# Kernel optimization log

Measured on AMD Instinct MI355X. Metric: run time of the kernel, lower is better.

The kernel has to match this reference:

```python
import jax, jax.numpy as jnp
import numpy as np

ALPHA = 0.2  # LeakyReLU negative slope
NEG = -9e15

def _gat_head(Wh, a1, a2, adj_mask):
    # Wh: [N,O], a1/a2: [O], adj_mask: [N,N] bool
    e = jax.nn.leaky_relu(jnp.einsum('no,o->n', Wh, a1)[:, None]
                          + jnp.einsum('no,o->n', Wh, a2)[None, :], ALPHA)
    att = jax.nn.softmax(jnp.where(adj_mask, e, NEG), axis=-1)
    return att @ Wh  # [N,O]

def setup_inputs() -> dict:
    key = jax.random.key(0)
    ks = jax.random.split(key, 6)
    N, F_IN, O, H, C = 4096, 512, 64, 8, 16
    x = jax.random.normal(ks[0], (N, F_IN), jnp.float32)
    adj = jax.random.randint(ks[1], (N, N), 0, 2, jnp.int32)
    W = jax.random.normal(ks[2], (H, F_IN, O), jnp.float32) * 0.05
    a = jax.random.normal(ks[3], (H, 2 * O), jnp.float32) * 0.05
    W_out = jax.random.normal(ks[4], (H * O, C), jnp.float32) * 0.05
    a_out = jax.random.normal(ks[5], (2 * C,), jnp.float32) * 0.05
    return {'x': x, 'adj': adj, 'W': W, 'a': a, 'W_out': W_out, 'a_out': a_out}

def reference(x, adj, W, a, W_out, a_out):
    N = x.shape[0]
    H, _, O = W.shape
    C = W_out.shape[1]
    mask = adj > 0  # [N,N]
    # multi-head attention layer (vmapped over heads)
    Wh = jnp.einsum('nf,hfo->hno', x, W)  # [H,N,O]
    a1, a2 = a[:, :O], a[:, O:]
    h_heads = jax.vmap(_gat_head, in_axes=(0, 0, 0, None))(Wh, a1, a2, mask)  # [H,N,O]
    h = jax.nn.elu(h_heads)  # concat=True -> elu per head
    h = jnp.transpose(h, (1, 0, 2)).reshape(N, H * O)  # concat heads
    # output attention layer (concat=False)
    Wh_o = h @ W_out  # [N,C]
    out = _gat_head(Wh_o, a_out[:C], a_out[C:], mask)  # [N,C]
    out = jax.nn.elu(out)
    return jax.nn.log_softmax(out, axis=1)
```

## Files before the change

### kernel.cpp

```cpp
#include <hip/hip_runtime.h>


typedef _Float16 h2 __attribute__((ext_vector_type(2)));
typedef _Float16 half8 __attribute__((ext_vector_type(8)));
typedef __attribute__((ext_vector_type(4))) float f32x4;
typedef unsigned long long u64;
typedef unsigned short u16;
typedef unsigned int u32;

__device__ __forceinline__ u16 f2h(float f){
  union { _Float16 h; u16 u; } c; c.h = (_Float16)f; return c.u;
}
__device__ __forceinline__ h2 u2h2(u32 u){ union { u32 u; h2 h; } c; c.u = u; return c.h; }
__device__ __forceinline__ u32 h22u(h2 h){ union { u32 u; h2 h; } c; c.h = h; return c.u; }
__device__ __forceinline__ half8 pk2h8(uint4 v){ union { uint4 u; half8 h; } c; c.u = v; return c.h; }

__device__ __forceinline__ void async16(void* lds, const void* g){
  __builtin_amdgcn_global_load_lds((const __attribute__((address_space(1))) u32*)g,
                                   (__attribute__((address_space(3))) u32*)lds, 16, 0, 0);
}
__device__ __forceinline__ void async4(void* lds, const void* g){
  __builtin_amdgcn_global_load_lds((const __attribute__((address_space(1))) u32*)g,
                                   (__attribute__((address_space(3))) u32*)lds, 4, 0, 0);
}

__global__ __launch_bounds__(256) void k_wpack(const float* __restrict__ W,
                                               u16* __restrict__ Wb16){
  int t = blockIdx.x * 256 + threadIdx.x;
  int o   = t & 63;
  int fgb = (t >> 6) & 63;
  int h   = t >> 12;
  const float* src = W + ((size_t)h * 512 + fgb * 8) * 64 + o;
  u32 pk[4];
  #pragma unroll
  for (int p = 0; p < 4; ++p)
    pk[p] = (u32)f2h(src[(2 * p) * 64]) | ((u32)f2h(src[(2 * p + 1) * 64]) << 16);
  *(uint4*)(Wb16 + ((size_t)h * 4096 + fgb * 64 + o) * 8) = *(uint4*)pk;
}

__global__ __launch_bounds__(256) void k_gemm1(const float* __restrict__ x,
                                               const u16* __restrict__ Wb16,
                                               const float* __restrict__ av,
                                               const int* __restrict__ adj,
                                               u16* __restrict__ whB,
                                               u64* __restrict__ bits_t,
                                               float* __restrict__ r1,
                                               u16* __restrict__ e21h, u16* __restrict__ e202h){
  __shared__ u16 tr[4096];
  int h    = blockIdx.y;
  int bx   = blockIdx.x;
  int tid  = threadIdx.x;
  int lane = tid & 63;
  int wv   = tid >> 6;

  if (bx >= 64){
    int B = h * 64 + (bx - 64);
    int uid0 = B * 512 + wv * 128;
    for (int k = 0; k < 128; k += 8){
      int v[8];
      #pragma unroll
      for (int q = 0; q < 8; ++q){
        int uid = uid0 + k + q;
        v[q] = adj[(size_t)(uid >> 6) * 4096 + ((uid & 63) << 6) + lane];
      }
      u64 m[8];
      #pragma unroll
      for (int q = 0; q < 8; ++q) m[q] = __ballot(v[q] != 0);
      if (lane == 0){
        #pragma unroll
        for (int q = 0; q < 8; ++q){
          int uid = uid0 + k + q;
          bits_t[(size_t)(uid & 63) * 4096 + (uid >> 6)] = m[q];
        }
      }
    }
    return;
  }

  int row16 = lane & 15, grp = lane >> 4;
  int n0 = bx * 64;
  int n0w = n0 + wv * 16;
  const u16* wb = Wb16 + (size_t)h * 32768;

  f32x4 acc[4] = {};
  #pragma unroll 4
  for (int ks = 0; ks < 16; ++ks){
    int fgb = ks * 4 + grp;
    const float* xs = x + (size_t)(n0w + row16) * 512 + fgb * 8;
    float4 xv0 = ((const float4*)xs)[0];
    float4 xv1 = ((const float4*)xs)[1];
    u32 ax[4];
    ax[0] = (u32)f2h(xv0.x) | ((u32)f2h(xv0.y) << 16);
    ax[1] = (u32)f2h(xv0.z) | ((u32)f2h(xv0.w) << 16);
    ax[2] = (u32)f2h(xv1.x) | ((u32)f2h(xv1.y) << 16);
    ax[3] = (u32)f2h(xv1.z) | ((u32)f2h(xv1.w) << 16);
    half8 af = pk2h8(*(uint4*)ax);
    #pragma unroll
    for (int nt = 0; nt < 4; ++nt){
      half8 bf = *(const half8*)(wb + ((size_t)fgb * 64 + nt * 16 + row16) * 8);
      acc[nt] = __builtin_amdgcn_mfma_f32_16x16x32_f16(af, bf, acc[nt], 0, 0, 0);
    }
  }
  float a1v[4], a2v[4];
  #pragma unroll
  for (int nt = 0; nt < 4; ++nt){
    a1v[nt] = av[h * 128 + nt * 16 + row16];
    a2v[nt] = av[h * 128 + 64 + nt * 16 + row16];
  }
  #pragma unroll
  for (int r = 0; r < 4; ++r){
    float p1 = acc[0][r]*a1v[0] + acc[1][r]*a1v[1] + acc[2][r]*a1v[2] + acc[3][r]*a1v[3];
    float p2 = acc[0][r]*a2v[0] + acc[1][r]*a2v[1] + acc[2][r]*a2v[2] + acc[3][r]*a2v[3];
    #pragma unroll
    for (int d = 1; d < 16; d <<= 1){ p1 += __shfl_xor(p1, d, 64); p2 += __shfl_xor(p2, d, 64); }
    if (row16 == 0){
      int idx = h * 4096 + n0w + grp * 4 + r;
      r1[idx]    = __expf(-0.8f * p1);
      e21h[idx]  = f2h(__expf(p2));
      e202h[idx] = f2h(__expf(0.2f * p2));
    }
  }
  #pragma unroll
  for (int nt = 0; nt < 4; ++nt)
    #pragma unroll
    for (int r = 0; r < 4; ++r){
      int jl = wv * 16 + grp * 4 + r;
      int o  = nt * 16 + row16;
      tr[((jl >> 3) * 64 + o) * 8 + (jl & 7)] = f2h(acc[nt][r]);
    }
  __syncthreads();
  u16* dst = whB + (size_t)h * 262144 + (size_t)n0 * 64;
  #pragma unroll
  for (int q = 0; q < 2; ++q)
    *(uint4*)(dst + (tid * 2 + q) * 8) = *(const uint4*)(tr + (tid * 2 + q) * 8);
}

__global__ __launch_bounds__(256) void k_att1(const u16* __restrict__ whB,
                                              const u64* __restrict__ bits_t,
                                              const float* __restrict__ r1,
                                              const u16* __restrict__ e21h, const u16* __restrict__ e202h,
                                              u16* __restrict__ pnum, float* __restrict__ pden){
  __shared__ u16  smB[2][4096];
  __shared__ u32  smT[2][2][64];
  __shared__ u32  smLut[4];
  int h     = blockIdx.y;
  int iblk  = blockIdx.x;
  int split = blockIdx.z;
  int lane = threadIdx.x & 63;
  int wv   = threadIdx.x >> 6;
  int row16 = lane & 15, grp = lane >> 4;
  if (threadIdx.x < 4)
    smLut[threadIdx.x] = ((threadIdx.x & 1) ? 0xFFFFu : 0u) | ((threadIdx.x & 2) ? 0xFFFF0000u : 0u);
  int i = iblk * 64 + wv * 16 + row16;
  int hoff = h * 4096;
  u32 rb = (u32)f2h(r1[hoff + i]); rb |= rb << 16;
  h2 rr = u2h2(rb);
  const u16* whBh = whB + (size_t)h * 262144;
  int jbeg = split * 1024;

  half8 bden;
  {
    u32 z[4] = {0,0,0,0};
    if (row16 == 0){ z[0]=0x3C003C00u; z[1]=0x3C003C00u; z[2]=0x3C003C00u; z[3]=0x3C003C00u; }
    bden = pk2h8(*(uint4*)z);
  }

  auto stage = [&](int bb, int j0){
    const char* g = (const char*)whBh + (size_t)j0 * 128 + wv * 2048 + lane * 16;
    char* l = (char*)(&smB[bb][0]) + wv * 2048;
    async16(l, g);
    async16(l + 1024, g + 1024);
    if (wv == 0)      async4(&smT[bb][0][0], (const char*)(e21h  + hoff + j0) + lane * 4);
    else if (wv == 1) async4(&smT[bb][1][0], (const char*)(e202h + hoff + j0) + lane * 4);
  };

  f32x4 acc[4] = {};
  f32x4 accden = {};
  stage(0, jbeg);
  for (int c = 0; c < 16; ++c){
    int bb = c & 1;
    u64 mrow = bits_t[(size_t)(split * 16 + c) * 4096 + i];
    __syncthreads();
    if (c < 15) stage(bb ^ 1, jbeg + (c + 1) * 64);
    #pragma unroll
    for (int ks = 0; ks < 2; ++ks){
      uint4 e1q = *(const uint4*)((const char*)&smT[bb][0][0] + ks * 64 + grp * 16);
      uint4 e2q = *(const uint4*)((const char*)&smT[bb][1][0] + ks * 64 + grp * 16);
      u32 es[4] = {e1q.x, e1q.y, e1q.z, e1q.w};
      u32 gs[4] = {e2q.x, e2q.y, e2q.z, e2q.w};
      const u16* bbase = &smB[bb][(ks * 4 + grp) * 512];
      half8 bf0 = *(const half8*)(bbase + (0 * 16 + row16) * 8);
      half8 bf1 = *(const half8*)(bbase + (1 * 16 + row16) * 8);
      half8 bf2 = *(const half8*)(bbase + (2 * 16 + row16) * 8);
      half8 bf3 = *(const half8*)(bbase + (3 * 16 + row16) * 8);
      u32 mb = ((u32)(mrow >> (ks * 32)) >> (grp * 8)) & 0xffu;
      u32 pk[4];
      #pragma unroll
      for (int t2i = 0; t2i < 4; ++t2i){
        h2 w = __builtin_elementwise_max(u2h2(es[t2i]), rr * u2h2(gs[t2i]));
        pk[t2i] = h22u(w) & smLut[(mb >> (2 * t2i)) & 3u];
      }
      half8 af = pk2h8(*(uint4*)pk);
      acc[0] = __builtin_amdgcn_mfma_f32_16x16x32_f16(af, bf0, acc[0], 0, 0, 0);
      acc[1] = __builtin_amdgcn_mfma_f32_16x16x32_f16(af, bf1, acc[1], 0, 0, 0);
      acc[2] = __builtin_amdgcn_mfma_f32_16x16x32_f16(af, bf2, acc[2], 0, 0, 0);
      acc[3] = __builtin_amdgcn_mfma_f32_16x16x32_f16(af, bf3, acc[3], 0, 0, 0);
      accden = __builtin_amdgcn_mfma_f32_16x16x32_f16(af, bden, accden, 0, 0, 0);
    }
  }

  #pragma unroll
  for (int r4 = 0; r4 < 4; ++r4){
    int n = iblk * 64 + wv * 16 + grp * 4 + r4;
    if (row16 == 0)
      pden[((size_t)split * 8 + h) * 4096 + n] = accden[r4];
    u16* dst = pnum + ((size_t)split * 4096 + n) * 512 + h * 64 + row16;
    #pragma unroll
    for (int nt = 0; nt < 4; ++nt)
      dst[nt * 16] = f2h(acc[nt][r4]);
  }
}

__global__ __launch_bounds__(256) void k_gemm2(const u16* __restrict__ pnum,
                                               const float* __restrict__ pden,
                                               const float* __restrict__ Wout,
                                               const float* __restrict__ aout,
                                               u16* __restrict__ whoB,
                                               float* __restrict__ r1o,
                                               u16* __restrict__ e21oh, u16* __restrict__ e202oh){
  __shared__ float Wl[8192];
  __shared__ float hrow[16 * 516];
  __shared__ float sden[128];
  int n0 = blockIdx.x * 16;
  for (int t = threadIdx.x; t < 8192; t += 256) Wl[t] = Wout[t];
  if (threadIdx.x < 128){
    int hh = threadIdx.x >> 4, nn = threadIdx.x & 15;
    float d = 0.f;
    #pragma unroll
    for (int s = 0; s < 4; ++s) d += pden[((size_t)s * 8 + hh) * 4096 + n0 + nn];
    sden[threadIdx.x] = d;
  }
  __syncthreads();
  {
    int nn = threadIdx.x >> 4;
    int fc = threadIdx.x & 15;
    int f0 = fc * 32;
    int hh = fc >> 1;
    float dinv = 1.f / sden[hh * 16 + nn];
    float v[32];
    #pragma unroll
    for (int k = 0; k < 32; ++k) v[k] = 0.f;
    #pragma unroll
    for (int s = 0; s < 4; ++s){
      const u16* p = pnum + ((size_t)s * 4096 + n0 + nn) * 512 + f0;
      #pragma unroll
      for (int q = 0; q < 4; ++q){
        uint4 raw = *(const uint4*)(p + q * 8);
        u32 rw[4] = {raw.x, raw.y, raw.z, raw.w};
        #pragma unroll
        for (int d2 = 0; d2 < 4; ++d2){
          h2 dh = u2h2(rw[d2]);
          v[q * 8 + d2 * 2]     += (float)dh.x;
          v[q * 8 + d2 * 2 + 1] += (float)dh.y;
        }
      }
    }
    #pragma unroll
    for (int k = 0; k < 32; ++k){
      float val = v[k] * dinv;
      val = val > 0.f ? val : (__expf(val) - 1.f);
      hrow[nn * 516 + f0 + k] = val;
    }
  }
  __syncthreads();
  int c  = threadIdx.x & 15;
  int rl = threadIdx.x >> 4;
  int n = n0 + rl;
  const float4* hr = (const float4*)(hrow + rl * 516);
  float acc = 0.f;
  #pragma unroll 8
  for (int f4 = 0; f4 < 128; ++f4){
    float4 hv = hr[f4];
    int f = f4 * 4;
    acc += hv.x * Wl[f * 16 + c] + hv.y * Wl[(f + 1) * 16 + c]
         + hv.z * Wl[(f + 2) * 16 + c] + hv.w * Wl[(f + 3) * 16 + c];
  }
  whoB[((size_t)(n >> 3) * 16 + c) * 8 + (n & 7)] = f2h(acc);
  float p1 = acc * aout[c], p2 = acc * aout[16 + c];
  #pragma unroll
  for (int d = 1; d < 16; d <<= 1){ p1 += __shfl_xor(p1, d, 64); p2 += __shfl_xor(p2, d, 64); }
  if (c == 0){
    r1o[n]    = __expf(-0.8f * p1);
    e21oh[n]  = f2h(__expf(p2));
    e202oh[n] = f2h(__expf(0.2f * p2));
  }
}

__global__ __launch_bounds__(256) void k_att2(const u16* __restrict__ whoB,
                                              const u64* __restrict__ bits_t,
                                              const float* __restrict__ r1o,
                                              const u16* __restrict__ e21oh, const u16* __restrict__ e202oh,
                                              float* __restrict__ pnum, float* __restrict__ pden){
  __shared__ u32 smLut[4];
  int iblk  = blockIdx.x;
  int split = blockIdx.y;
  int lane = threadIdx.x & 63;
  int wv   = threadIdx.x >> 6;
  int row16 = lane & 15, grp = lane >> 4;
  if (threadIdx.x < 4)
    smLut[threadIdx.x] = ((threadIdx.x & 1) ? 0xFFFFu : 0u) | ((threadIdx.x & 2) ? 0xFFFF0000u : 0u);
  __syncthreads();
  int i = iblk * 64 + wv * 16 + row16;
  u32 rb = (u32)f2h(r1o[i]); rb |= rb << 16;
  h2 rr = u2h2(rb);
  int jbeg = split * 256;
  half8 bden;
  {
    u32 z[4] = {0,0,0,0};
    if (row16 == 0){ z[0]=0x3C003C00u; z[1]=0x3C003C00u; z[2]=0x3C003C00u; z[3]=0x3C003C00u; }
    bden = pk2h8(*(uint4*)z);
  }

  f32x4 acc = {};
  f32x4 accden = {};
  #pragma unroll
  for (int c = 0; c < 4; ++c){
    int j0 = jbeg + c * 64;
    u64 mrow = bits_t[(size_t)(split * 4 + c) * 4096 + i];
    #pragma unroll
    for (int ks = 0; ks < 2; ++ks){
      int sb = (j0 >> 3) + ks * 4 + grp;
      half8 bf = *(const half8*)(whoB + ((size_t)sb * 16 + row16) * 8);
      uint4 e1q = *(const uint4*)(e21oh  + j0 + ks * 32 + grp * 8);
      uint4 e2q = *(const uint4*)(e202oh + j0 + ks * 32 + grp * 8);
      u32 es[4] = {e1q.x, e1q.y, e1q.z, e1q.w};
      u32 gs[4] = {e2q.x, e2q.y, e2q.z, e2q.w};
      u32 mb = ((u32)(mrow >> (ks * 32)) >> (grp * 8)) & 0xffu;
      u32 pk[4];
      #pragma unroll
      for (int t2i = 0; t2i < 4; ++t2i){
        h2 w = __builtin_elementwise_max(u2h2(es[t2i]), rr * u2h2(gs[t2i]));
        pk[t2i] = h22u(w) & smLut[(mb >> (2 * t2i)) & 3u];
      }
      half8 af = pk2h8(*(uint4*)pk);
      acc    = __builtin_amdgcn_mfma_f32_16x16x32_f16(af, bf, acc, 0, 0, 0);
      accden = __builtin_amdgcn_mfma_f32_16x16x32_f16(af, bden, accden, 0, 0, 0);
    }
  }
  #pragma unroll
  for (int r4 = 0; r4 < 4; ++r4){
    int n = iblk * 64 + wv * 16 + grp * 4 + r4;
    if (row16 == 0)
      pden[(size_t)n * 16 + split] = accden[r4];
    pnum[((size_t)n * 16 + split) * 16 + row16] = acc[r4];
  }
}

__global__ __launch_bounds__(256) void k_final(const float* __restrict__ pnum,
                                               const float* __restrict__ pden,
                                               float* __restrict__ out){
  int tid = blockIdx.x * 256 + threadIdx.x;
  int c = tid & 15;
  int n = tid >> 4;
  float num = 0.f, den = 0.f;
  #pragma unroll
  for (int s = 0; s < 16; ++s){
    num += pnum[((size_t)n * 16 + s) * 16 + c];
    den += pden[(size_t)n * 16 + s];
  }
  float v = num / den;
  v = v > 0.f ? v : (__expf(v) - 1.f);
  float m = v;
  #pragma unroll
  for (int d = 1; d < 16; d <<= 1) m = fmaxf(m, __shfl_xor(m, d, 64));
  float es = __expf(v - m), ss = es;
  #pragma unroll
  for (int d = 1; d < 16; d <<= 1) ss += __shfl_xor(ss, d, 64);
  out[(size_t)n * 16 + c] = v - m - __logf(ss);
}

extern "C" void kernel_launch(void* const* d_in, const int* in_sizes, int n_in,
                              void* d_out, int out_size, void* d_ws, size_t ws_size,
                              hipStream_t stream){
  (void)in_sizes; (void)n_in; (void)out_size; (void)ws_size;
  const float* x    = (const float*)d_in[0];
  const int*   adj  = (const int*)d_in[1];
  const float* W    = (const float*)d_in[2];
  const float* av   = (const float*)d_in[3];
  const float* Wout = (const float*)d_in[4];
  const float* aout = (const float*)d_in[5];
  float* out = (float*)d_out;
  char* ws = (char*)d_ws;

  u64*  bits_t  = (u64*)(ws + 0x0000000);
  u16*  whB     = (u16*)(ws + 0x0200000);
  float* r1     = (float*)(ws + 0x0600000);
  u16*  e21h    = (u16*)(ws + 0x0620000);
  u16*  e202h   = (u16*)(ws + 0x0630000);
  u16*  pnum1   = (u16*)(ws + 0x0680000);
  float* pden1  = (float*)(ws + 0x1680000);
  u16*  whoB    = (u16*)(ws + 0x1700000);
  float* r1o    = (float*)(ws + 0x1720000);
  u16*  e21oh   = (u16*)(ws + 0x1724000);
  u16*  e202oh  = (u16*)(ws + 0x1726000);
  float* pnum2  = (float*)(ws + 0x1730000);
  float* pden2  = (float*)(ws + 0x1B30000);
  u16*  Wb16    = (u16*)(ws + 0x1730000);

  k_wpack<<<dim3(128), dim3(256), 0, stream>>>(W, Wb16);
  k_gemm1<<<dim3(128, 8), dim3(256), 0, stream>>>(x, Wb16, av, adj, whB, bits_t, r1, e21h, e202h);
  k_att1<<<dim3(64, 8, 4), dim3(256), 0, stream>>>(whB, bits_t, r1, e21h, e202h, pnum1, pden1);
  k_gemm2<<<dim3(256), dim3(256), 0, stream>>>(pnum1, pden1, Wout, aout, whoB, r1o, e21oh, e202oh);
  k_att2<<<dim3(64, 16), dim3(256), 0, stream>>>(whoB, bits_t, r1o, e21oh, e202oh, pnum2, pden2);
  k_final<<<dim3(256), dim3(256), 0, stream>>>(pnum2, pden2, out);
}
```

Baseline: 175.3 us.

## Pre-pack x to fp16 MFMA layout and restructure gemm2 as one row per wave

```diff
diff --git a/kernel.cpp b/kernel.cpp
--- a/kernel.cpp
+++ b/kernel.cpp
@@ -24,21 +24,44 @@
                                    (__attribute__((address_space(3))) u32*)lds, 4, 0, 0);
 }
 
-__global__ __launch_bounds__(256) void k_wpack(const float* __restrict__ W,
-                                               u16* __restrict__ Wb16){
-  int t = blockIdx.x * 256 + threadIdx.x;
-  int o   = t & 63;
-  int fgb = (t >> 6) & 63;
-  int h   = t >> 12;
-  const float* src = W + ((size_t)h * 512 + fgb * 8) * 64 + o;
-  u32 pk[4];
-  #pragma unroll
-  for (int p = 0; p < 4; ++p)
-    pk[p] = (u32)f2h(src[(2 * p) * 64]) | ((u32)f2h(src[(2 * p + 1) * 64]) << 16);
-  *(uint4*)(Wb16 + ((size_t)h * 4096 + fgb * 64 + o) * 8) = *(uint4*)pk;
-}
-
-__global__ __launch_bounds__(256) void k_gemm1(const float* __restrict__ x,
+__global__ __launch_bounds__(256) void k_prep(const float* __restrict__ W,
+                                              const float* __restrict__ x,
+                                              u16* __restrict__ Wb16,
+                                              u16* __restrict__ xA){
+  int bx = blockIdx.x;
+  int tid = threadIdx.x;
+  if (bx < 256){
+    int ngrp = bx;
+    int row16 = tid & 15;
+    int fq    = tid >> 4;
+    const float* xs = x + ((size_t)ngrp * 16 + row16) * 512;
+    #pragma unroll
+    for (int it = 0; it < 4; ++it){
+      int fgb = fq * 4 + it;
+      float4 a0 = *(const float4*)(xs + fgb * 8);
+      float4 a1 = *(const float4*)(xs + fgb * 8 + 4);
+      u32 pk[4];
+      pk[0] = (u32)f2h(a0.x) | ((u32)f2h(a0.y) << 16);
+      pk[1] = (u32)f2h(a0.z) | ((u32)f2h(a0.w) << 16);
+      pk[2] = (u32)f2h(a1.x) | ((u32)f2h(a1.y) << 16);
+      pk[3] = (u32)f2h(a1.z) | ((u32)f2h(a1.w) << 16);
+      *(uint4*)(xA + (((size_t)ngrp * 64 + fgb) * 16 + row16) * 8) = *(uint4*)pk;
+    }
+  } else {
+    int t = (bx - 256) * 256 + tid;
+    int o   = t & 63;
+    int fgb = (t >> 6) & 63;
+    int h   = t >> 12;
+    const float* src = W + ((size_t)h * 512 + fgb * 8) * 64 + o;
+    u32 pk[4];
+    #pragma unroll
+    for (int p = 0; p < 4; ++p)
+      pk[p] = (u32)f2h(src[(2 * p) * 64]) | ((u32)f2h(src[(2 * p + 1) * 64]) << 16);
+    *(uint4*)(Wb16 + ((size_t)h * 4096 + fgb * 64 + o) * 8) = *(uint4*)pk;
+  }
+}
+
+__global__ __launch_bounds__(256) void k_gemm1(const u16* __restrict__ xA,
                                                const u16* __restrict__ Wb16,
                                                const float* __restrict__ av,
                                                const int* __restrict__ adj,
@@ -81,20 +104,13 @@
   int n0 = bx * 64;
   int n0w = n0 + wv * 16;
   const u16* wb = Wb16 + (size_t)h * 32768;
+  const u16* xa = xA + (size_t)(bx * 4 + wv) * 8192;
 
   f32x4 acc[4] = {};
   #pragma unroll 4
   for (int ks = 0; ks < 16; ++ks){
     int fgb = ks * 4 + grp;
-    const float* xs = x + (size_t)(n0w + row16) * 512 + fgb * 8;
-    float4 xv0 = ((const float4*)xs)[0];
-    float4 xv1 = ((const float4*)xs)[1];
-    u32 ax[4];
-    ax[0] = (u32)f2h(xv0.x) | ((u32)f2h(xv0.y) << 16);
-    ax[1] = (u32)f2h(xv0.z) | ((u32)f2h(xv0.w) << 16);
-    ax[2] = (u32)f2h(xv1.x) | ((u32)f2h(xv1.y) << 16);
-    ax[3] = (u32)f2h(xv1.z) | ((u32)f2h(xv1.w) << 16);
-    half8 af = pk2h8(*(uint4*)ax);
+    half8 af = *(const half8*)(xa + ((size_t)fgb * 16 + row16) * 8);
     #pragma unroll
     for (int nt = 0; nt < 4; ++nt){
       half8 bf = *(const half8*)(wb + ((size_t)fgb * 64 + nt * 16 + row16) * 8);
@@ -228,68 +244,57 @@
                                                u16* __restrict__ whoB,
                                                float* __restrict__ r1o,
                                                u16* __restrict__ e21oh, u16* __restrict__ e202oh){
-  __shared__ float Wl[8192];
-  __shared__ float hrow[16 * 516];
-  __shared__ float sden[128];
-  int n0 = blockIdx.x * 16;
-  for (int t = threadIdx.x; t < 8192; t += 256) Wl[t] = Wout[t];
-  if (threadIdx.x < 128){
-    int hh = threadIdx.x >> 4, nn = threadIdx.x & 15;
-    float d = 0.f;
-    #pragma unroll
-    for (int s = 0; s < 4; ++s) d += pden[((size_t)s * 8 + hh) * 4096 + n0 + nn];
-    sden[threadIdx.x] = d;
-  }
-  __syncthreads();
-  {
-    int nn = threadIdx.x >> 4;
-    int fc = threadIdx.x & 15;
-    int f0 = fc * 32;
-    int hh = fc >> 1;
-    float dinv = 1.f / sden[hh * 16 + nn];
-    float v[32];
-    #pragma unroll
-    for (int k = 0; k < 32; ++k) v[k] = 0.f;
-    #pragma unroll
-    for (int s = 0; s < 4; ++s){
-      const u16* p = pnum + ((size_t)s * 4096 + n0 + nn) * 512 + f0;
-      #pragma unroll
-      for (int q = 0; q < 4; ++q){
-        uint4 raw = *(const uint4*)(p + q * 8);
-        u32 rw[4] = {raw.x, raw.y, raw.z, raw.w};
-        #pragma unroll
-        for (int d2 = 0; d2 < 4; ++d2){
-          h2 dh = u2h2(rw[d2]);
-          v[q * 8 + d2 * 2]     += (float)dh.x;
-          v[q * 8 + d2 * 2 + 1] += (float)dh.y;
-        }
-      }
-    }
-    #pragma unroll
-    for (int k = 0; k < 32; ++k){
-      float val = v[k] * dinv;
-      val = val > 0.f ? val : (__expf(val) - 1.f);
-      hrow[nn * 516 + f0 + k] = val;
-    }
-  }
-  __syncthreads();
-  int c  = threadIdx.x & 15;
-  int rl = threadIdx.x >> 4;
-  int n = n0 + rl;
-  const float4* hr = (const float4*)(hrow + rl * 516);
-  float acc = 0.f;
-  #pragma unroll 8
-  for (int f4 = 0; f4 < 128; ++f4){
-    float4 hv = hr[f4];
-    int f = f4 * 4;
-    acc += hv.x * Wl[f * 16 + c] + hv.y * Wl[(f + 1) * 16 + c]
-         + hv.z * Wl[(f + 2) * 16 + c] + hv.w * Wl[(f + 3) * 16 + c];
-  }
-  whoB[((size_t)(n >> 3) * 16 + c) * 8 + (n & 7)] = f2h(acc);
-  float p1 = acc * aout[c], p2 = acc * aout[16 + c];
-  #pragma unroll
-  for (int d = 1; d < 16; d <<= 1){ p1 += __shfl_xor(p1, d, 64); p2 += __shfl_xor(p2, d, 64); }
-  if (c == 0){
+  int wv = threadIdx.x >> 6;
+  int l  = threadIdx.x & 63;
+  int n  = blockIdx.x * 4 + wv;
+  int f0 = l * 8;
+  int hh = l >> 3;
+  float v[8] = {0.f,0.f,0.f,0.f,0.f,0.f,0.f,0.f};
+  float d = 0.f;
+  #pragma unroll
+  for (int s = 0; s < 4; ++s){
+    uint4 raw = *(const uint4*)(pnum + ((size_t)s * 4096 + n) * 512 + f0);
+    u32 rw[4] = {raw.x, raw.y, raw.z, raw.w};
+    #pragma unroll
+    for (int q = 0; q < 4; ++q){
+      h2 dh = u2h2(rw[q]);
+      v[q * 2]     += (float)dh.x;
+      v[q * 2 + 1] += (float)dh.y;
+    }
+    d += pden[((size_t)s * 8 + hh) * 4096 + n];
+  }
+  float dinv = 1.f / d;
+  #pragma unroll
+  for (int k = 0; k < 8; ++k){
+    float val = v[k] * dinv;
+    v[k] = val > 0.f ? val : (__expf(val) - 1.f);
+  }
+  float pc[16];
+  #pragma unroll
+  for (int c = 0; c < 16; ++c) pc[c] = 0.f;
+  const float4* wr = (const float4*)(Wout + (size_t)f0 * 16);
+  #pragma unroll
+  for (int k = 0; k < 8; ++k){
+    float4 w0 = wr[k * 4 + 0], w1 = wr[k * 4 + 1], w2 = wr[k * 4 + 2], w3 = wr[k * 4 + 3];
+    float vk = v[k];
+    pc[0]  += vk * w0.x;  pc[1]  += vk * w0.y;  pc[2]  += vk * w0.z;  pc[3]  += vk * w0.w;
+    pc[4]  += vk * w1.x;  pc[5]  += vk * w1.y;  pc[6]  += vk * w1.z;  pc[7]  += vk * w1.w;
+    pc[8]  += vk * w2.x;  pc[9]  += vk * w2.y;  pc[10] += vk * w2.z;  pc[11] += vk * w2.w;
+    pc[12] += vk * w3.x;  pc[13] += vk * w3.y;  pc[14] += vk * w3.z;  pc[15] += vk * w3.w;
+  }
+  #pragma unroll
+  for (int c = 0; c < 16; ++c)
+    #pragma unroll
+    for (int dd = 1; dd < 64; dd <<= 1)
+      pc[c] += __shfl_xor(pc[c], dd, 64);
+  if (l == 0){
+    float p1 = 0.f, p2 = 0.f;
+    #pragma unroll
+    for (int c = 0; c < 16; ++c){
+      whoB[((size_t)(n >> 3) * 16 + c) * 8 + (n & 7)] = f2h(pc[c]);
+      p1 += pc[c] * aout[c];
+      p2 += pc[c] * aout[16 + c];
+    }
     r1o[n]    = __expf(-0.8f * p1);
     e21oh[n]  = f2h(__expf(p2));
     e202oh[n] = f2h(__expf(0.2f * p2));
@@ -406,11 +411,12 @@
   float* pnum2  = (float*)(ws + 0x1730000);
   float* pden2  = (float*)(ws + 0x1B30000);
   u16*  Wb16    = (u16*)(ws + 0x1730000);
-
-  k_wpack<<<dim3(128), dim3(256), 0, stream>>>(W, Wb16);
-  k_gemm1<<<dim3(128, 8), dim3(256), 0, stream>>>(x, Wb16, av, adj, whB, bits_t, r1, e21h, e202h);
+  u16*  xA      = (u16*)(ws + 0x0680000);
+
+  k_prep<<<dim3(384), dim3(256), 0, stream>>>(W, x, Wb16, xA);
+  k_gemm1<<<dim3(128, 8), dim3(256), 0, stream>>>(xA, Wb16, av, adj, whB, bits_t, r1, e21h, e202h);
   k_att1<<<dim3(64, 8, 4), dim3(256), 0, stream>>>(whB, bits_t, r1, e21h, e202h, pnum1, pden1);
-  k_gemm2<<<dim3(256), dim3(256), 0, stream>>>(pnum1, pden1, Wout, aout, whoB, r1o, e21oh, e202oh);
+  k_gemm2<<<dim3(1024), dim3(256), 0, stream>>>(pnum1, pden1, Wout, aout, whoB, r1o, e21oh, e202oh);
   k_att2<<<dim3(64, 16), dim3(256), 0, stream>>>(whoB, bits_t, r1o, e21oh, e202oh, pnum2, pden2);
   k_final<<<dim3(256), dim3(256), 0, stream>>>(pnum2, pden2, out);
 }
```

Result: slower. 186.0 us (+6.1%).

## Restructure gemm2 to four rows per block with split-K and direct W_out reads

Applied to the files above, without the earlier changes.

```diff
diff --git a/kernel.cpp b/kernel.cpp
--- a/kernel.cpp
+++ b/kernel.cpp
@@ -228,68 +228,59 @@
                                                u16* __restrict__ whoB,
                                                float* __restrict__ r1o,
                                                u16* __restrict__ e21oh, u16* __restrict__ e202oh){
-  __shared__ float Wl[8192];
-  __shared__ float hrow[16 * 516];
-  __shared__ float sden[128];
-  int n0 = blockIdx.x * 16;
-  for (int t = threadIdx.x; t < 8192; t += 256) Wl[t] = Wout[t];
-  if (threadIdx.x < 128){
-    int hh = threadIdx.x >> 4, nn = threadIdx.x & 15;
+  __shared__ float hrowf[4][512];
+  int n0  = blockIdx.x * 4;
+  int tid = threadIdx.x;
+  {
+    int nn = tid >> 6;
+    int fc = tid & 63;
+    int f0 = fc * 8;
+    int hh = fc >> 3;
+    int n  = n0 + nn;
+    float v[8] = {0.f,0.f,0.f,0.f,0.f,0.f,0.f,0.f};
     float d = 0.f;
     #pragma unroll
-    for (int s = 0; s < 4; ++s) d += pden[((size_t)s * 8 + hh) * 4096 + n0 + nn];
-    sden[threadIdx.x] = d;
-  }
-  __syncthreads();
-  {
-    int nn = threadIdx.x >> 4;
-    int fc = threadIdx.x & 15;
-    int f0 = fc * 32;
-    int hh = fc >> 1;
-    float dinv = 1.f / sden[hh * 16 + nn];
-    float v[32];
-    #pragma unroll
-    for (int k = 0; k < 32; ++k) v[k] = 0.f;
-    #pragma unroll
     for (int s = 0; s < 4; ++s){
-      const u16* p = pnum + ((size_t)s * 4096 + n0 + nn) * 512 + f0;
+      uint4 raw = *(const uint4*)(pnum + ((size_t)s * 4096 + n) * 512 + f0);
+      u32 rw[4] = {raw.x, raw.y, raw.z, raw.w};
       #pragma unroll
       for (int q = 0; q < 4; ++q){
-        uint4 raw = *(const uint4*)(p + q * 8);
-        u32 rw[4] = {raw.x, raw.y, raw.z, raw.w};
-        #pragma unroll
-        for (int d2 = 0; d2 < 4; ++d2){
-          h2 dh = u2h2(rw[d2]);
-          v[q * 8 + d2 * 2]     += (float)dh.x;
-          v[q * 8 + d2 * 2 + 1] += (float)dh.y;
-        }
+        h2 dh = u2h2(rw[q]);
+        v[q * 2]     += (float)dh.x;
+        v[q * 2 + 1] += (float)dh.y;
       }
-    }
-    #pragma unroll
-    for (int k = 0; k < 32; ++k){
+      d += pden[((size_t)s * 8 + hh) * 4096 + n];
+    }
+    float dinv = 1.f / d;
+    #pragma unroll
+    for (int k = 0; k < 8; ++k){
       float val = v[k] * dinv;
-      val = val > 0.f ? val : (__expf(val) - 1.f);
-      hrow[nn * 516 + f0 + k] = val;
+      hrowf[nn][f0 + k] = val > 0.f ? val : (__expf(val) - 1.f);
     }
   }
   __syncthreads();
-  int c  = threadIdx.x & 15;
-  int rl = threadIdx.x >> 4;
-  int n = n0 + rl;
-  const float4* hr = (const float4*)(hrow + rl * 516);
-  float acc = 0.f;
-  #pragma unroll 8
-  for (int f4 = 0; f4 < 128; ++f4){
-    float4 hv = hr[f4];
-    int f = f4 * 4;
-    acc += hv.x * Wl[f * 16 + c] + hv.y * Wl[(f + 1) * 16 + c]
-         + hv.z * Wl[(f + 2) * 16 + c] + hv.w * Wl[(f + 3) * 16 + c];
-  }
-  whoB[((size_t)(n >> 3) * 16 + c) * 8 + (n & 7)] = f2h(acc);
+  int rl = tid >> 6;
+  int kq = (tid >> 4) & 3;
+  int c  = tid & 15;
+  int n  = n0 + rl;
+  const float* hr = &hrowf[rl][kq * 128];
+  const float* wp = Wout + (size_t)(kq * 128) * 16 + c;
+  float a0 = 0.f, a1 = 0.f;
+  #pragma unroll 16
+  for (int f = 0; f < 128; f += 2){
+    a0 += hr[f]     * wp[f * 16];
+    a1 += hr[f + 1] * wp[f * 16 + 16];
+  }
+  float acc = a0 + a1;
+  acc += __shfl_xor(acc, 16, 64);
+  acc += __shfl_xor(acc, 32, 64);
+  int lane = tid & 63;
+  if ((lane >> 4) == 0)
+    whoB[((size_t)(n >> 3) * 16 + c) * 8 + (n & 7)] = f2h(acc);
   float p1 = acc * aout[c], p2 = acc * aout[16 + c];
   #pragma unroll
   for (int d = 1; d < 16; d <<= 1){ p1 += __shfl_xor(p1, d, 64); p2 += __shfl_xor(p2, d, 64); }
-  if (c == 0){
+  if (lane == 0){
     r1o[n]    = __expf(-0.8f * p1);
     e21oh[n]  = f2h(__expf(p2));
     e202oh[n] = f2h(__expf(0.2f * p2));
@@ -410,7 +401,7 @@
   k_wpack<<<dim3(128), dim3(256), 0, stream>>>(W, Wb16);
   k_gemm1<<<dim3(128, 8), dim3(256), 0, stream>>>(x, Wb16, av, adj, whB, bits_t, r1, e21h, e202h);
   k_att1<<<dim3(64, 8, 4), dim3(256), 0, stream>>>(whB, bits_t, r1, e21h, e202h, pnum1, pden1);
-  k_gemm2<<<dim3(256), dim3(256), 0, stream>>>(pnum1, pden1, Wout, aout, whoB, r1o, e21oh, e202oh);
+  k_gemm2<<<dim3(1024), dim3(256), 0, stream>>>(pnum1, pden1, Wout, aout, whoB, r1o, e21oh, e202oh);
   k_att2<<<dim3(64, 16), dim3(256), 0, stream>>>(whoB, bits_t, r1o, e21oh, e202oh, pnum2, pden2);
   k_final<<<dim3(256), dim3(256), 0, stream>>>(pnum2, pden2, out);
 }
```

After: 174.4 us. Within noise of the previous version (-0.5%).
